# Kernel tuning notes

Measured on AMD Instinct MI355X. Metric: run time of the kernel, lower is better.

## Reference

```python
import jax, jax.numpy as jnp
import numpy as np

B, T, INPUT_DIM = 4, 2048, 1024
DIM, H = 64, 16  # per-head dim, n_heads


def setup_inputs() -> dict:
    key = jax.random.key(0)
    k1, k2, k3, k4 = jax.random.split(key, 4)
    x = jax.random.normal(k1, (B, T, INPUT_DIM), dtype=jnp.float32)
    # nn.Linear(input_dim, 3*h*d, bias=False)
    w_qkv = jax.random.normal(k2, (INPUT_DIM, 3 * H * DIM), dtype=jnp.float32) * (INPUT_DIM ** -0.5)
    # nn.Linear(h*d, input_dim) with bias
    w_out = jax.random.normal(k3, (H * DIM, INPUT_DIM), dtype=jnp.float32) * ((H * DIM) ** -0.5)
    b_out = jax.random.normal(k4, (INPUT_DIM,), dtype=jnp.float32) * 0.01
    return {"x": x, "w_qkv": w_qkv, "w_out": w_out, "b_out": b_out}


def reference(x, w_qkv, w_out, b_out):
    b, t, _ = x.shape
    scale = DIM ** -0.5
    qkv = x @ w_qkv                                   # [b, t, 3*h*d]
    # 'b t (qkv h d) -> qkv b h t d'
    qkv = qkv.reshape(b, t, 3, H, DIM)
    qkv = jnp.transpose(qkv, (2, 0, 3, 1, 4))         # [3, b, h, t, d]
    q, k, v = qkv[0], qkv[1], qkv[2]
    dot = jnp.einsum('bhtd,bhkd->bhtk', q, k) * scale # [b, h, t, t]
    att = jax.nn.softmax(dot, axis=-1)
    out = jnp.einsum('bhtk,bhkd->bhtd', att, v)       # [b, h, t, d]
    out = jnp.transpose(out, (0, 2, 1, 3)).reshape(b, t, H * DIM)
    return out @ w_out + b_out
```

## Files before the change

### kernel.cpp

```cpp
#include <hip/hip_runtime.h>
#include <hip/hip_bf16.h>
#include <stdint.h>

typedef __attribute__((ext_vector_type(8))) short bf16x8;
typedef __attribute__((ext_vector_type(4))) short s16x4;
typedef __attribute__((ext_vector_type(4))) float f32x4;

__device__ __forceinline__ void mfma_bf16(f32x4& c, bf16x8 a, bf16x8 b) {
  asm("v_mfma_f32_16x16x32_bf16 %0, %1, %2, %0" : "+v"(c) : "v"(a), "v"(b));
}

__device__ __forceinline__ void gload_lds16(const void* g, void* lds) {
  __builtin_amdgcn_global_load_lds(
      (const __attribute__((address_space(1))) void*)g,
      (__attribute__((address_space(3))) void*)lds, 16, 0, 0);
}

__global__ void cvt_f32_bf16(const float* __restrict__ in, __hip_bfloat16* __restrict__ out, int n4) {
  int i = blockIdx.x * blockDim.x + threadIdx.x;
  if (i >= n4) return;
  float4 v = reinterpret_cast<const float4*>(in)[i];
  __hip_bfloat162 a = __float22bfloat162_rn(make_float2(v.x, v.y));
  __hip_bfloat162 b = __float22bfloat162_rn(make_float2(v.z, v.w));
  reinterpret_cast<__hip_bfloat162*>(out)[i * 2]     = a;
  reinterpret_cast<__hip_bfloat162*>(out)[i * 2 + 1] = b;
}

__global__ void transpose_cvt(const float* __restrict__ in, __hip_bfloat16* __restrict__ out,
                              int R, int C) {
  __shared__ float tile[32][33];
  int c0 = blockIdx.x * 32, r0 = blockIdx.y * 32;
#pragma unroll
  for (int k = 0; k < 4; k++)
    tile[threadIdx.y + 8 * k][threadIdx.x] =
        in[(size_t)(r0 + threadIdx.y + 8 * k) * C + c0 + threadIdx.x];
  __syncthreads();
#pragma unroll
  for (int k = 0; k < 4; k++)
    out[(size_t)(c0 + threadIdx.y + 8 * k) * R + r0 + threadIdx.x] =
        __float2bfloat16(tile[threadIdx.x][threadIdx.y + 8 * k]);
}

template <int MODE>
__global__ __launch_bounds__(256) void gemm_bf16(
    const __hip_bfloat16* __restrict__ A, const __hip_bfloat16* __restrict__ Bt,
    int M, int N, int K,
    __hip_bfloat16* __restrict__ qb, __hip_bfloat16* __restrict__ kb,
    __hip_bfloat16* __restrict__ vt,
    float* __restrict__ outp, const float* __restrict__ bias) {
  constexpr int BK = 32;
  __shared__ __align__(16) __hip_bfloat16 As[128 * BK];
  __shared__ __align__(16) __hip_bfloat16 Bs[128 * BK];
  const int tid = threadIdx.x;
  const int wave = tid >> 6, lane = tid & 63;
  const int wr = wave >> 1, wc = wave & 1;
  const int m0 = blockIdx.y * 128;
  const int n0 = (MODE == 2 ? 2048 : 0) + blockIdx.x * 128;

  f32x4 acc[4][4];
#pragma unroll
  for (int i = 0; i < 4; i++)
#pragma unroll
    for (int j = 0; j < 4; j++) acc[i][j] = (f32x4)(0.0f);

  const int c0 = wave * 2, c1 = c0 + 1;
  const int srow0 = c0 * 16 + (lane >> 2);
  const int srow1 = c1 * 16 + (lane >> 2);
  const int scol = (lane & 3) * 8;
  const __hip_bfloat16* Ag0 = A + (size_t)(m0 + srow0) * K + scol;
  const __hip_bfloat16* Ag1 = A + (size_t)(m0 + srow1) * K + scol;
  const __hip_bfloat16* Bg0 = Bt + (size_t)(n0 + srow0) * K + scol;
  const __hip_bfloat16* Bg1 = Bt + (size_t)(n0 + srow1) * K + scol;
  __hip_bfloat16* AsP0 = &As[c0 * 512];
  __hip_bfloat16* AsP1 = &As[c1 * 512];
  __hip_bfloat16* BsP0 = &Bs[c0 * 512];
  __hip_bfloat16* BsP1 = &Bs[c1 * 512];

  for (int kk = 0; kk < K; kk += BK) {
    gload_lds16(Ag0 + kk, AsP0);
    gload_lds16(Ag1 + kk, AsP1);
    gload_lds16(Bg0 + kk, BsP0);
    gload_lds16(Bg1 + kk, BsP1);
    __syncthreads();
    bf16x8 af[4], bfr[4];
#pragma unroll
    for (int i = 0; i < 4; i++)
      af[i] = *(const bf16x8*)&As[(wr * 64 + i * 16 + (lane & 15)) * BK + (lane >> 4) * 8];
#pragma unroll
    for (int j = 0; j < 4; j++)
      bfr[j] = *(const bf16x8*)&Bs[(wc * 64 + j * 16 + (lane & 15)) * BK + (lane >> 4) * 8];
#pragma unroll
    for (int i = 0; i < 4; i++)
#pragma unroll
      for (int j = 0; j < 4; j++) {
        if constexpr (MODE == 2)
          mfma_bf16(acc[i][j], bfr[j], af[i]);
        else
          mfma_bf16(acc[i][j], af[i], bfr[j]);
      }
    __syncthreads();
  }

  if constexpr (MODE == 0) {
#pragma unroll
    for (int j = 0; j < 4; j++) {
      int col = n0 + wc * 64 + j * 16 + (lane & 15);
      int sel = col >> 10;
      int h = (col >> 6) & 15;
      int d = col & 63;
      __hip_bfloat16* dst = sel ? kb : qb;
      float scl = sel ? 1.0f : 0.125f;
#pragma unroll
      for (int i = 0; i < 4; i++) {
#pragma unroll
        for (int r = 0; r < 4; r++) {
          int row = m0 + wr * 64 + i * 16 + (lane >> 4) * 4 + r;
          int b = row >> 11, t = row & 2047;
          dst[(((size_t)b * 16 + h) * 2048 + t) * 64 + d] = __float2bfloat16(acc[i][j][r] * scl);
        }
      }
    }
  } else if constexpr (MODE == 2) {
#pragma unroll
    for (int j = 0; j < 4; j++) {
#pragma unroll
      for (int r = 0; r < 4; r++) {
        int nrow = n0 + wc * 64 + j * 16 + (lane >> 4) * 4 + r;
        int h = (nrow >> 6) & 15;
        int d = nrow & 63;
#pragma unroll
        for (int i = 0; i < 4; i++) {
          int tcol = m0 + wr * 64 + i * 16 + (lane & 15);
          int b = tcol >> 11, t = tcol & 2047;
          vt[(((size_t)b * 16 + h) * 64 + d) * 2048 + t] = __float2bfloat16(acc[i][j][r]);
        }
      }
    }
  } else {
#pragma unroll
    for (int j = 0; j < 4; j++) {
      int col = n0 + wc * 64 + j * 16 + (lane & 15);
      float bv = bias[col];
#pragma unroll
      for (int i = 0; i < 4; i++) {
#pragma unroll
        for (int r = 0; r < 4; r++) {
          int row = m0 + wr * 64 + i * 16 + (lane >> 4) * 4 + r;
          outp[(size_t)row * N + col] = acc[i][j][r] + bv;
        }
      }
    }
  }
}

__global__ __launch_bounds__(256) void attn_fwd(
    const __hip_bfloat16* __restrict__ Qb, const __hip_bfloat16* __restrict__ Kb,
    const __hip_bfloat16* __restrict__ Vtg, __hip_bfloat16* __restrict__ Ob) {
  constexpr int T = 2048;
  __shared__ __align__(16) __hip_bfloat16 Ks[2][4096];
  __shared__ __align__(16) __hip_bfloat16 Vs[2][4096];
  __shared__ __align__(16) __hip_bfloat16 Ps[4][1024];
  const int tid = threadIdx.x, wave = tid >> 6, lane = tid & 63;

  int id = ((int)blockIdx.x & 7) * 256 + ((int)blockIdx.x >> 3);
  const int bh = id >> 5, q0 = (id & 31) * 64;
  const size_t baseQ = (size_t)bh * T * 64;
  const size_t baseV = (size_t)bh * 64 * T;

  bf16x8 qf[2];
  {
    const int qrow = q0 + wave * 16 + (lane & 15);
#pragma unroll
    for (int ks = 0; ks < 2; ks++)
      qf[ks] = *(const bf16x8*)&Qb[baseQ + (size_t)qrow * 64 + ks * 32 + (lane >> 4) * 8];
  }

  float m_run = -3.0e38f, l_run = 0.0f;
  f32x4 o[4];
#pragma unroll
  for (int fd = 0; fd < 4; fd++) o[fd] = (f32x4)(0.0f);

  const int sr = lane >> 3;
  const int q8 = (lane & 7) ^ sr;
  const char* KgB = (const char*)(Kb + baseQ);
  const char* VgB = (const char*)(Vtg + baseV);
  const int cc0 = wave * 2, cc1 = cc0 + 1;
  char* PwB = (char*)&Ps[wave][0];
  const int prow = lane & 15, hi = lane >> 4;

#define STAGE(kt, buf)                                                                   \
  do {                                                                                   \
    char* kd = (char*)Ks[buf];                                                           \
    char* vd = (char*)Vs[buf];                                                           \
    gload_lds16(KgB + (size_t)((kt) * 64 + cc0 * 8 + sr) * 128 + q8 * 16, kd + cc0 * 1024); \
    gload_lds16(KgB + (size_t)((kt) * 64 + cc1 * 8 + sr) * 128 + q8 * 16, kd + cc1 * 1024); \
    gload_lds16(VgB + (size_t)(cc0 * 8 + sr) * 4096 + (kt) * 128 + q8 * 16, vd + cc0 * 1024); \
    gload_lds16(VgB + (size_t)(cc1 * 8 + sr) * 4096 + (kt) * 128 + q8 * 16, vd + cc1 * 1024); \
  } while (0)

  STAGE(0, 0);
  int cur = 0;

  for (int kt = 0; kt < T / 64; kt++) {
    if (kt < T / 64 - 1) {
      STAGE(kt + 1, cur ^ 1);
      asm volatile("s_waitcnt vmcnt(4)" ::: "memory");
    } else {
      asm volatile("s_waitcnt vmcnt(0)" ::: "memory");
    }
    __builtin_amdgcn_s_barrier();
    __builtin_amdgcn_sched_barrier(0);
    const char* KsB = (const char*)Ks[cur];
    const char* VtB = (const char*)Vs[cur];

    f32x4 s[4];
#pragma unroll
    for (int kf = 0; kf < 4; kf++) s[kf] = (f32x4)(0.0f);
#pragma unroll
    for (int ks = 0; ks < 2; ks++) {
#pragma unroll
      for (int kf = 0; kf < 4; kf++) {
        int key = kf * 16 + prow;
        int byteoff = (key * 128 + ks * 64 + hi * 16) ^ ((key & 7) << 4);
        bf16x8 kfrag = *(const bf16x8*)(KsB + byteoff);
        mfma_bf16(s[kf], kfrag, qf[ks]);
      }
    }

    float tm = s[0][0];
#pragma unroll
    for (int kf = 0; kf < 4; kf++)
#pragma unroll
      for (int r = 0; r < 4; r++) tm = fmaxf(tm, s[kf][r]);
    tm = fmaxf(tm, __shfl_xor(tm, 16));
    tm = fmaxf(tm, __shfl_xor(tm, 32));
    float mn = fmaxf(m_run, tm);
    float alpha = __expf(m_run - mn);
    m_run = mn;
    float rs = 0.0f;
    float p[4][4];
#pragma unroll
    for (int kf = 0; kf < 4; kf++)
#pragma unroll
      for (int r = 0; r < 4; r++) {
        float pv = __expf(s[kf][r] - mn);
        p[kf][r] = pv;
        rs += pv;
      }
    rs += __shfl_xor(rs, 16);
    rs += __shfl_xor(rs, 32);
    l_run = l_run * alpha + rs;

#pragma unroll
    for (int r = 0; r < 4; r++) {
      float ar = __shfl(alpha, hi * 4 + r);
#pragma unroll
      for (int fd = 0; fd < 4; fd++) o[fd][r] *= ar;
    }

#pragma unroll
    for (int kf = 0; kf < 4; kf++) {
      s16x4 pk;
      pk.x = (short)__bfloat16_as_short(__float2bfloat16(p[kf][0]));
      pk.y = (short)__bfloat16_as_short(__float2bfloat16(p[kf][1]));
      pk.z = (short)__bfloat16_as_short(__float2bfloat16(p[kf][2]));
      pk.w = (short)__bfloat16_as_short(__float2bfloat16(p[kf][3]));
      int wb = (prow * 128 + kf * 32 + hi * 8) ^ ((prow & 7) << 4);
      *(s16x4*)(PwB + wb) = pk;
    }

#pragma unroll
    for (int ks = 0; ks < 2; ks++) {
      int pbyte = (prow * 128 + ks * 64 + hi * 16) ^ ((prow & 7) << 4);
      bf16x8 pa = *(const bf16x8*)(PwB + pbyte);
#pragma unroll
      for (int fd = 0; fd < 4; fd++) {
        int d = fd * 16 + prow;
        int vbyte = (d * 128 + ks * 64 + hi * 16) ^ ((d & 7) << 4);
        bf16x8 vf = *(const bf16x8*)(VtB + vbyte);
        mfma_bf16(o[fd], pa, vf);
      }
    }
    __builtin_amdgcn_sched_barrier(0);
    __builtin_amdgcn_s_barrier();
    cur ^= 1;
  }
#undef STAGE

  const int b = bh >> 4, h = bh & 15;
#pragma unroll
  for (int r = 0; r < 4; r++) {
    float lr = __shfl(l_run, hi * 4 + r);
    float inv = 1.0f / lr;
    int trow = q0 + wave * 16 + hi * 4 + r;
#pragma unroll
    for (int fd = 0; fd < 4; fd++) {
      int col = h * 64 + fd * 16 + prow;
      Ob[((size_t)(b * 2048 + trow)) * 1024 + col] = __float2bfloat16(o[fd][r] * inv);
    }
  }
}

extern "C" void kernel_launch(void* const* d_in, const int* in_sizes, int n_in,
                              void* d_out, int out_size, void* d_ws, size_t ws_size,
                              hipStream_t stream) {
  const float* x = (const float*)d_in[0];
  const float* w_qkv = (const float*)d_in[1];
  const float* w_out = (const float*)d_in[2];
  const float* b_out = (const float*)d_in[3];
  float* out = (float*)d_out;

  size_t need = (size_t)37748736 * 2;
  if (ws_size < need) return;
  __hip_bfloat16* wsp = (__hip_bfloat16*)d_ws;
  __hip_bfloat16* x_bf = wsp;
  __hip_bfloat16* wqkv_t = x_bf + 8192 * 1024;
  __hip_bfloat16* wout_t = wqkv_t + 3072 * 1024;
  __hip_bfloat16* qb = wout_t + 1024 * 1024;
  __hip_bfloat16* kb = qb + 8388608;
  __hip_bfloat16* vt = kb + 8388608;
  __hip_bfloat16* ab = x_bf;

  cvt_f32_bf16<<<8192, 256, 0, stream>>>(x, x_bf, 8192 * 1024 / 4);
  transpose_cvt<<<dim3(3072 / 32, 1024 / 32), dim3(32, 8), 0, stream>>>(w_qkv, wqkv_t, 1024, 3072);
  transpose_cvt<<<dim3(1024 / 32, 1024 / 32), dim3(32, 8), 0, stream>>>(w_out, wout_t, 1024, 1024);
  gemm_bf16<0><<<dim3(16, 64), 256, 0, stream>>>(x_bf, wqkv_t, 8192, 3072, 1024,
                                                 qb, kb, nullptr, nullptr, nullptr);
  gemm_bf16<2><<<dim3(8, 64), 256, 0, stream>>>(x_bf, wqkv_t, 8192, 3072, 1024,
                                                nullptr, nullptr, vt, nullptr, nullptr);
  attn_fwd<<<2048, 256, 0, stream>>>(qb, kb, vt, ab);
  gemm_bf16<1><<<dim3(8, 64), 256, 0, stream>>>(ab, wout_t, 8192, 1024, 1024,
                                                nullptr, nullptr, nullptr, out, b_out);
}
```

Measured before the change: 247.4 us.

## Use exp2 with pre-folded log2e, lazy rescaling, deferred row-sum reduction in attention

Folds log2(e) into the Q scale so softmax exponentials can use exp2 directly. Skips the running-max update and output rescale unless some lane's tile max exceeds the old max by more than a threshold. Defers the cross-lane row-sum shuffles to the end of the kernel, packs P conversion with paired bf16 intrinsics, and raises wave priority around the MFMA blocks. The intent is to cut VALU and shuffle work per tile, at the cost of exponentials that can grow up to 2^11.5 before rescaling.

Result: no change. 249.6 us (+0.9%).

```diff
diff --git a/kernel.cpp b/kernel.cpp
--- a/kernel.cpp
+++ b/kernel.cpp
@@ -109,7 +109,7 @@
       int h = (col >> 6) & 15;
       int d = col & 63;
       __hip_bfloat16* dst = sel ? kb : qb;
-      float scl = sel ? 1.0f : 0.125f;
+      float scl = sel ? 1.0f : 0.18033688f;
 #pragma unroll
       for (int i = 0; i < 4; i++) {
 #pragma unroll
@@ -157,6 +157,7 @@
     const __hip_bfloat16* __restrict__ Qb, const __hip_bfloat16* __restrict__ Kb,
     const __hip_bfloat16* __restrict__ Vtg, __hip_bfloat16* __restrict__ Ob) {
   constexpr int T = 2048;
+  constexpr float THR = 11.5f;
   __shared__ __align__(16) __hip_bfloat16 Ks[2][4096];
   __shared__ __align__(16) __hip_bfloat16 Vs[2][4096];
   __shared__ __align__(16) __hip_bfloat16 Ps[4][1024];
@@ -175,7 +176,8 @@
       qf[ks] = *(const bf16x8*)&Qb[baseQ + (size_t)qrow * 64 + ks * 32 + (lane >> 4) * 8];
   }
 
-  float m_run = -3.0e38f, l_run = 0.0f;
+  float m_run = -3.0e38f;
+  float l_part = 0.0f;
   f32x4 o[4];
 #pragma unroll
   for (int fd = 0; fd < 4; fd++) o[fd] = (f32x4)(0.0f);
@@ -216,6 +218,7 @@
     f32x4 s[4];
 #pragma unroll
     for (int kf = 0; kf < 4; kf++) s[kf] = (f32x4)(0.0f);
+    __builtin_amdgcn_s_setprio(1);
 #pragma unroll
     for (int ks = 0; ks < 2; ks++) {
 #pragma unroll
@@ -226,49 +229,50 @@
         mfma_bf16(s[kf], kfrag, qf[ks]);
       }
     }
-
-    float tm = s[0][0];
-#pragma unroll
-    for (int kf = 0; kf < 4; kf++)
-#pragma unroll
-      for (int r = 0; r < 4; r++) tm = fmaxf(tm, s[kf][r]);
+    __builtin_amdgcn_s_setprio(0);
+
+    float t0 = fmaxf(fmaxf(s[0][0], s[0][1]), s[0][2]);
+    float t1 = fmaxf(fmaxf(s[0][3], s[1][0]), s[1][1]);
+    float t2 = fmaxf(fmaxf(s[1][2], s[1][3]), s[2][0]);
+    float t3 = fmaxf(fmaxf(s[2][1], s[2][2]), s[2][3]);
+    float t4 = fmaxf(fmaxf(s[3][0], s[3][1]), s[3][2]);
+    float tm = fmaxf(fmaxf(fmaxf(t0, t1), t2), fmaxf(fmaxf(t3, t4), s[3][3]));
     tm = fmaxf(tm, __shfl_xor(tm, 16));
     tm = fmaxf(tm, __shfl_xor(tm, 32));
-    float mn = fmaxf(m_run, tm);
-    float alpha = __expf(m_run - mn);
-    m_run = mn;
-    float rs = 0.0f;
-    float p[4][4];
-#pragma unroll
-    for (int kf = 0; kf < 4; kf++)
+
+    if (!__all(tm - m_run <= THR)) {
+      float mn = fmaxf(m_run, tm);
+      float alpha = __builtin_exp2f(m_run - mn);
+      m_run = mn;
+      l_part *= alpha;
 #pragma unroll
       for (int r = 0; r < 4; r++) {
-        float pv = __expf(s[kf][r] - mn);
-        p[kf][r] = pv;
-        rs += pv;
-      }
-    rs += __shfl_xor(rs, 16);
-    rs += __shfl_xor(rs, 32);
-    l_run = l_run * alpha + rs;
-
-#pragma unroll
-    for (int r = 0; r < 4; r++) {
-      float ar = __shfl(alpha, hi * 4 + r);
-#pragma unroll
-      for (int fd = 0; fd < 4; fd++) o[fd][r] *= ar;
-    }
-
+        float ar = __shfl(alpha, hi * 4 + r);
+#pragma unroll
+        for (int fd = 0; fd < 4; fd++) o[fd][r] *= ar;
+      }
+    }
+
+    float rs0 = 0.0f, rs1 = 0.0f;
 #pragma unroll
     for (int kf = 0; kf < 4; kf++) {
-      s16x4 pk;
-      pk.x = (short)__bfloat16_as_short(__float2bfloat16(p[kf][0]));
-      pk.y = (short)__bfloat16_as_short(__float2bfloat16(p[kf][1]));
-      pk.z = (short)__bfloat16_as_short(__float2bfloat16(p[kf][2]));
-      pk.w = (short)__bfloat16_as_short(__float2bfloat16(p[kf][3]));
+      float p0 = __builtin_exp2f(s[kf][0] - m_run);
+      float p1 = __builtin_exp2f(s[kf][1] - m_run);
+      float p2 = __builtin_exp2f(s[kf][2] - m_run);
+      float p3 = __builtin_exp2f(s[kf][3] - m_run);
+      rs0 += p0 + p1;
+      rs1 += p2 + p3;
+      __hip_bfloat162 h01 = __float22bfloat162_rn(make_float2(p0, p1));
+      __hip_bfloat162 h23 = __float22bfloat162_rn(make_float2(p2, p3));
+      int2 w;
+      w.x = *(int*)&h01;
+      w.y = *(int*)&h23;
       int wb = (prow * 128 + kf * 32 + hi * 8) ^ ((prow & 7) << 4);
-      *(s16x4*)(PwB + wb) = pk;
-    }
-
+      *(int2*)(PwB + wb) = w;
+    }
+    l_part += rs0 + rs1;
+
+    __builtin_amdgcn_s_setprio(1);
 #pragma unroll
     for (int ks = 0; ks < 2; ks++) {
       int pbyte = (prow * 128 + ks * 64 + hi * 16) ^ ((prow & 7) << 4);
@@ -281,12 +285,16 @@
         mfma_bf16(o[fd], pa, vf);
       }
     }
+    __builtin_amdgcn_s_setprio(0);
     __builtin_amdgcn_sched_barrier(0);
     __builtin_amdgcn_s_barrier();
     cur ^= 1;
   }
 #undef STAGE
 
+  float l_run = l_part;
+  l_run += __shfl_xor(l_run, 16);
+  l_run += __shfl_xor(l_run, 32);
   const int b = bh >> 4, h = bh & 15;
 #pragma unroll
   for (int r = 0; r < 4; r++) {
```
